# Kernel optimization log

Hardware: AMD Instinct MI355X
Metric: run time of the kernel (lower is better)

The kernel has to match this reference:

```python
import jax, jax.numpy as jnp
from jax import lax
import numpy as np

EPS = 1e-5

def _bn(x, g, b, m, v):
    # inference-mode BatchNorm2d over channel dim (NCHW)
    scale = (g * lax.rsqrt(v + EPS))[None, :, None, None]
    return (x - m[None, :, None, None]) * scale + b[None, :, None, None]

def _conv(x, w, dil, pad):
    return lax.conv_general_dilated(
        x, w, window_strides=(1, 1), padding=[(pad, pad), (pad, pad)],
        rhs_dilation=(dil, dil), dimension_numbers=('NCHW', 'OIHW', 'NCHW'))

def _interleave(b0, b1, b2, b3):
    # out[2i+r, 2j+c] = branch[2r+c][i, j]  (equivalent to the mask*nearest-upsample trick)
    bs, C, H, W = b0.shape
    row0 = jnp.stack([b0, b1], axis=-1)          # (bs,C,H,W,2) -> c
    row1 = jnp.stack([b2, b3], axis=-1)
    s = jnp.stack([row0, row1], axis=-2)          # (bs,C,H,W,2,2) -> (...,r,c)
    return s.transpose(0, 1, 2, 4, 3, 5).reshape(bs, C, 2 * H, 2 * W)

def setup_inputs() -> dict:
    key = jax.random.key(0)
    ks = iter(jax.random.split(key, 40))
    B, Cin, Cout, H = 8, 256, 128, 64
    inp = {"x": jax.random.normal(next(ks), (B, Cin, H, H), jnp.float32)}
    inp["w0"] = jax.random.normal(next(ks), (Cout, Cin, 1, 1), jnp.float32) * 0.05
    for i in (1, 2, 3):
        inp[f"w{i}"] = jax.random.normal(next(ks), (Cout, Cin, 3, 3), jnp.float32) * 0.02
    inp["wp"] = jax.random.normal(next(ks), (Cout, Cout, 1, 1), jnp.float32) * 0.05
    for t in ("0", "1", "2", "3", "p"):
        inp[f"g{t}"] = 1.0 + 0.1 * jax.random.normal(next(ks), (Cout,), jnp.float32)
        inp[f"b{t}"] = 0.1 * jax.random.normal(next(ks), (Cout,), jnp.float32)
        inp[f"m{t}"] = 0.05 * jax.random.normal(next(ks), (Cout,), jnp.float32)
        inp[f"v{t}"] = jax.random.uniform(next(ks), (Cout,), jnp.float32, 0.5, 1.5)
    return inp

def reference(x, w0, w1, w2, w3, wp,
              g0, b0, m0, v0, g1, b1, m1, v1,
              g2, b2, m2, v2, g3, b3, m3, v3,
              gp, bp, mp, vp):
    RATES = (6, 12, 18)
    br0 = jax.nn.relu(_bn(_conv(x, w0, 1, 0), g0, b0, m0, v0))
    br1 = jax.nn.relu(_bn(_conv(x, w1, RATES[0], RATES[0]), g1, b1, m1, v1))
    br2 = jax.nn.relu(_bn(_conv(x, w2, RATES[1], RATES[1]), g2, b2, m2, v2))
    br3 = jax.nn.relu(_bn(_conv(x, w3, RATES[2], RATES[2]), g3, b3, m3, v3))
    up = _interleave(br0, br1, br2, br3)          # (B, Cout, 2H, 2W)
    return jax.nn.relu(_bn(_conv(up, wp, 1, 0), gp, bp, mp, vp))  # dropout: eval identity
```

## Files before the change

### kernel.cpp

```cpp
#include <hip/hip_runtime.h>
#include <stdint.h>

typedef unsigned int uint32;
typedef uint16_t u16;
typedef short short8 __attribute__((ext_vector_type(8)));
typedef short shortx4 __attribute__((ext_vector_type(4)));
typedef float floatx4 __attribute__((ext_vector_type(4)));

#define BN_EPS 1e-5f

#define XROW 25600
#define XPLANE 1638400
#define XB_SHORTS 13107200
#define ZROW_SHORTS 25600

#define OFF0 0
#define OFF1 32768
#define OFF2 327680
#define OFF3 622592
#define OFFP 917504
#define WPK_SHORTS 933888
#define U_B0 4096
#define U_B  36864
#define U_TOT 116736

__device__ __forceinline__ u16 f2bf(float f) {
  uint32 u = __float_as_uint(f);
  u += 0x7fffu + ((u >> 16) & 1u);
  return (u16)(u >> 16);
}

__global__ void k_xcvt(const float* __restrict__ x, u16* __restrict__ xb) {
  int bid = blockIdx.x, tid = threadIdx.x;
  if (bid == 512) {
    uint32* z = (uint32*)(xb + XB_SHORTS);
    #pragma unroll
    for (int r = 0; r < 50; ++r) z[r * 256 + tid] = 0;
    return;
  }
  int n = bid >> 6, i = bid & 63;
  uint32* rw = (uint32*)(xb + (size_t)n * XPLANE + (size_t)i * XROW);
  #pragma unroll
  for (int e = 0; e < 18; ++e) {
    int idx = e * 256 + tid;
    int colid = idx >> 7;
    int jp = (colid < 18) ? colid : (colid + 64);
    rw[jp * 128 + (idx & 127)] = 0;
  }
  int ci2 = tid & 127, jh = tid >> 7;
  const float* xs = x + ((size_t)(n * 256 + 2 * ci2) * 64 + i) * 64 + jh * 32;
  #pragma unroll 4
  for (int j = 0; j < 32; ++j) {
    float f0 = xs[j];
    float f1 = xs[4096 + j];
    uint32 pk = (uint32)f2bf(f0) | ((uint32)f2bf(f1) << 16);
    rw[(jh * 32 + j + 18) * 128 + ci2] = pk;
  }
}

__global__ void k_wpack(const float* __restrict__ w0, const float* __restrict__ w1,
                        const float* __restrict__ w2, const float* __restrict__ w3,
                        const float* __restrict__ wp, u16* __restrict__ wpk) {
  int g = blockIdx.x * 256 + threadIdx.x;
  if (g >= U_TOT) return;
  const float* w; int Cin, t, q, u, off; bool k3;
  if (g < U_B0) {
    int blk = g >> 10; w = w0; Cin = 256; k3 = false; t = 0; q = blk; u = g & 1023;
    off = OFF0 + blk * 8192;
  } else if (g < U_B0 + U_B) {
    int g1 = g - U_B0; int blk = g1 >> 10; w = w1; Cin = 256; k3 = true;
    t = blk >> 2; q = blk & 3; u = g1 & 1023; off = OFF1 + blk * 8192;
  } else if (g < U_B0 + 2*U_B) {
    int g1 = g - (U_B0 + U_B); int blk = g1 >> 10; w = w2; Cin = 256; k3 = true;
    t = blk >> 2; q = blk & 3; u = g1 & 1023; off = OFF2 + blk * 8192;
  } else if (g < U_B0 + 3*U_B) {
    int g1 = g - (U_B0 + 2*U_B); int blk = g1 >> 10; w = w3; Cin = 256; k3 = true;
    t = blk >> 2; q = blk & 3; u = g1 & 1023; off = OFF3 + blk * 8192;
  } else {
    int g1 = g - (U_B0 + 3*U_B); int blk = g1 >> 10; w = wp; Cin = 128; k3 = false;
    t = 0; q = blk; u = g1 & 1023; off = OFFP + blk * 8192;
  }
  int co = u >> 3, slot = u & 7;
  int sl = slot ^ (co & 7);
  int ci0 = q * 64 + sl * 8;
  int kh = k3 ? (t / 3) : 0, kw = k3 ? (t % 3) : 0;
  union { short8 s; u16 us[8]; } v;
  #pragma unroll
  for (int e = 0; e < 8; ++e) {
    int ci = ci0 + e;
    float wv = k3 ? w[((co * Cin + ci) * 3 + kh) * 3 + kw] : w[co * Cin + ci];
    v.us[e] = f2bf(wv);
  }
  *(short8*)(wpk + off + u * 8) = v.s;
}

__global__ void k_bn(const float* g0,const float* b0,const float* m0,const float* v0,
                     const float* g1,const float* b1,const float* m1,const float* v1,
                     const float* g2,const float* b2,const float* m2,const float* v2,
                     const float* g3,const float* b3,const float* m3,const float* v3,
                     const float* gp,const float* bp,const float* mp,const float* vp,
                     float* __restrict__ bn) {
  int i = blockIdx.x * 256 + threadIdx.x;
  if (i >= 640) return;
  int t = i >> 7, co = i & 127;
  const float *G, *B, *M, *V;
  if      (t == 0) { G=g0; B=b0; M=m0; V=v0; }
  else if (t == 1) { G=g1; B=b1; M=m1; V=v1; }
  else if (t == 2) { G=g2; B=b2; M=m2; V=v2; }
  else if (t == 3) { G=g3; B=b3; M=m3; V=v3; }
  else             { G=gp; B=bp; M=mp; V=vp; }
  float s = G[co] * rsqrtf(V[co] + BN_EPS);
  bn[t * 256 + co]       = s;
  bn[t * 256 + 128 + co] = B[co] - M[co] * s;
}

__global__ __launch_bounds__(256, 3)
void k_main(const u16* __restrict__ xb, const u16* __restrict__ wpk,
            const float* __restrict__ bn, float* __restrict__ out) {
  __shared__ __align__(16) u16 As[8192];
  __shared__ __align__(16) u16 BP[16384];

  int tid = threadIdx.x;
  int bid = blockIdx.x;
  int n = bid & 7;
  int rest = bid >> 3;
  int tile = rest >> 2;
  int b = (rest ^ (rest >> 5)) & 3;
  int i0 = tile * 2;
  int lane = tid & 63, wid = tid >> 6;
  int wm = wid >> 1, wn = wid & 1;
  int m16 = lane & 15, hh = lane >> 4;

  const u16* xg = xb + (size_t)n * XPLANE;
  const u16* zr = xb + XB_SHORTS;
  int d = (b == 0) ? 0 : ((b == 1) ? 6 : ((b == 2) ? 12 : 18));
  int NS = ((b == 0) ? 1 : 9) * 4;
  int woff8 = ((b == 0) ? OFF0 : (b == 1) ? OFF1 : (b == 2) ? OFF2 : OFF3) / 8;

  const short8* wpk8 = (const short8*)wpk;
  short8* AsS8 = (short8*)As;
  short8* BsS8 = (short8*)BP;
  const short8* PsS8 = (const short8*)BP;

  floatx4 acc[4][4];
  #pragma unroll
  for (int a1 = 0; a1 < 4; ++a1)
    #pragma unroll
    for (int a2 = 0; a2 < 4; ++a2) acc[a1][a2] = (floatx4){0.f, 0.f, 0.f, 0.f};

  short8 ra[4];
  short8 rb[4];
  int cg = tid & 7, pxo = tid >> 3;

  auto prefetch = [&](int s) {
    int abase = woff8 + s * 1024;
    #pragma unroll
    for (int w = 0; w < 4; ++w) ra[w] = wpk8[abase + w * 256 + tid];
    int t = s >> 2, q = s & 3;
    int di = d * (t / 3 - 1);
    int dj = d * (t % 3 - 1);
    #pragma unroll
    for (int k = 0; k < 4; ++k) {
      int px = k * 32 + pxo;
      int ii = i0 + (k >> 1) + di;
      const u16* base = (ii >= 0 && ii < 64) ? (xg + ii * XROW) : zr;
      int jj = (px & 63) + 18 + dj;
      rb[k] = *(const short8*)(base + jj * 256 + q * 64 + cg * 8);
    }
  };

  prefetch(0);

  for (int s = 0; s < NS; ++s) {
    __builtin_amdgcn_s_barrier();
    #pragma unroll
    for (int w = 0; w < 4; ++w) AsS8[w * 256 + tid] = ra[w];
    #pragma unroll
    for (int k = 0; k < 4; ++k) {
      int px = k * 32 + pxo;
      BsS8[px * 8 + (cg ^ (px & 7))] = rb[k];
    }
    if (s + 1 < NS) prefetch(s + 1);
    asm volatile("s_waitcnt lgkmcnt(0)" ::: "memory");
    __builtin_amdgcn_s_barrier();
    __builtin_amdgcn_sched_barrier(0);
    #pragma unroll
    for (int kk = 0; kk < 2; ++kk) {
      short8 af[4], bfr[4];
      #pragma unroll
      for (int f = 0; f < 4; ++f) {
        int row = wm * 64 + f * 16 + m16;
        af[f] = AsS8[row * 8 + ((kk * 4 + hh) ^ (row & 7))];
      }
      #pragma unroll
      for (int f = 0; f < 4; ++f) {
        int px = wn * 64 + f * 16 + m16;
        bfr[f] = BsS8[px * 8 + ((kk * 4 + hh) ^ (px & 7))];
      }
      #pragma unroll
      for (int fm = 0; fm < 4; ++fm)
        #pragma unroll
        for (int fn = 0; fn < 4; ++fn)
          acc[fm][fn] = __builtin_amdgcn_mfma_f32_16x16x32_bf16(
              af[fm], bfr[fn], acc[fm][fn], 0, 0, 0);
    }
  }

  __syncthreads();
  #pragma unroll
  for (int fm = 0; fm < 4; ++fm) {
    int co_base = wm * 64 + fm * 16 + hh * 4;
    float sc[4], sh[4];
    #pragma unroll
    for (int r = 0; r < 4; ++r) {
      sc[r] = bn[b * 256 + co_base + r];
      sh[r] = bn[b * 256 + 128 + co_base + r];
    }
    #pragma unroll
    for (int fn = 0; fn < 4; ++fn) {
      int px = wn * 64 + fn * 16 + m16;
      int sw = (px >> 1) & 7;
      int slot = (co_base >> 3) ^ sw;
      union { shortx4 s4; u16 us[4]; } pk;
      #pragma unroll
      for (int r = 0; r < 4; ++r)
        pk.us[r] = f2bf(fmaxf(acc[fm][fn][r] * sc[r] + sh[r], 0.f));
      *(shortx4*)&BP[px * 128 + slot * 8 + (co_base & 7)] = pk.s4;
    }
  }

  floatx4 acc2[4][4];
  #pragma unroll
  for (int a1 = 0; a1 < 4; ++a1)
    #pragma unroll
    for (int a2 = 0; a2 < 4; ++a2) acc2[a1][a2] = (floatx4){0.f, 0.f, 0.f, 0.f};

  for (int q = 0; q < 2; ++q) {
    if (q == 1) __syncthreads();
    int abase = OFFP / 8 + q * 1024;
    #pragma unroll
    for (int w = 0; w < 4; ++w) AsS8[w * 256 + tid] = wpk8[abase + w * 256 + tid];
    __syncthreads();
    #pragma unroll
    for (int kk = 0; kk < 2; ++kk) {
      short8 af[4], bfr[4];
      #pragma unroll
      for (int f = 0; f < 4; ++f) {
        int row = wm * 64 + f * 16 + m16;
        af[f] = AsS8[row * 8 + ((kk * 4 + hh) ^ (row & 7))];
      }
      #pragma unroll
      for (int f = 0; f < 4; ++f) {
        int px = wn * 64 + f * 16 + m16;
        int slot = q * 8 + kk * 4 + hh;
        bfr[f] = PsS8[px * 16 + (slot ^ ((px >> 1) & 7))];
      }
      #pragma unroll
      for (int fm = 0; fm < 4; ++fm)
        #pragma unroll
        for (int fn = 0; fn < 4; ++fn)
          acc2[fm][fn] = __builtin_amdgcn_mfma_f32_16x16x32_bf16(
              af[fm], bfr[fn], acc2[fm][fn], 0, 0, 0);
    }
  }

  int rb2 = b >> 1, cb = b & 1;
  #pragma unroll
  for (int fm = 0; fm < 4; ++fm) {
    #pragma unroll
    for (int r = 0; r < 4; ++r) {
      int co = wm * 64 + fm * 16 + hh * 4 + r;
      float s  = bn[1024 + co];
      float sh = bn[1024 + 128 + co];
      #pragma unroll
      for (int fn = 0; fn < 4; ++fn) {
        int px = wn * 64 + fn * 16 + m16;
        int i = i0 + (px >> 6), j = px & 63;
        float v = fmaxf(acc2[fm][fn][r] * s + sh, 0.f);
        out[(((n * 128 + co) * 128) + (2 * i + rb2)) * 128 + (2 * j + cb)] = v;
      }
    }
  }
}

extern "C" void kernel_launch(void* const* d_in, const int* in_sizes, int n_in,
                              void* d_out, int out_size, void* d_ws, size_t ws_size,
                              hipStream_t stream) {
  const float* x  = (const float*)d_in[0];
  const float* w0 = (const float*)d_in[1];
  const float* w1 = (const float*)d_in[2];
  const float* w2 = (const float*)d_in[3];
  const float* w3 = (const float*)d_in[4];
  const float* wp = (const float*)d_in[5];

  u16* xbuf = (u16*)d_ws;
  u16* wpk  = (u16*)d_ws + (XB_SHORTS + ZROW_SHORTS);
  float* bn = (float*)((char*)d_ws + (size_t)(XB_SHORTS + ZROW_SHORTS + WPK_SHORTS) * 2);

  k_xcvt<<<513, 256, 0, stream>>>(x, xbuf);
  k_wpack<<<456, 256, 0, stream>>>(w0, w1, w2, w3, wp, wpk);
  k_bn<<<3, 256, 0, stream>>>(
      (const float*)d_in[6],  (const float*)d_in[7],  (const float*)d_in[8],  (const float*)d_in[9],
      (const float*)d_in[10], (const float*)d_in[11], (const float*)d_in[12], (const float*)d_in[13],
      (const float*)d_in[14], (const float*)d_in[15], (const float*)d_in[16], (const float*)d_in[17],
      (const float*)d_in[18], (const float*)d_in[19], (const float*)d_in[20], (const float*)d_in[21],
      (const float*)d_in[22], (const float*)d_in[23], (const float*)d_in[24], (const float*)d_in[25],
      bn);
  k_main<<<1024, 256, 0, stream>>>(xbuf, wpk, bn, (float*)d_out);
}
```

Before: 109.2 us.

## Load weight MFMA fragments directly from global memory, dropping the LDS A tile

The weight packing layout changes to slot-major order so each lane can fetch its MFMA A fragments straight from global memory (L2-resident weights). The A operand no longer goes through LDS in either the conv GEMM loop or the projection GEMM, which removes the LDS As buffer, its stores and reads, and some barriers. This frees 16KB of LDS, which could raise occupancy. In exchange the global weight loads are issued inside the loop without a full stage of prefetch, so latency may be exposed. The sched_barrier is also removed.

```diff
diff --git a/kernel.cpp b/kernel.cpp
--- a/kernel.cpp
+++ b/kernel.cpp
@@ -80,9 +80,8 @@
     int g1 = g - (U_B0 + 3*U_B); int blk = g1 >> 10; w = wp; Cin = 128; k3 = false;
     t = 0; q = blk; u = g1 & 1023; off = OFFP + blk * 8192;
   }
-  int co = u >> 3, slot = u & 7;
-  int sl = slot ^ (co & 7);
-  int ci0 = q * 64 + sl * 8;
+  int slot = u >> 7, co = u & 127;
+  int ci0 = q * 64 + slot * 8;
   int kh = k3 ? (t / 3) : 0, kw = k3 ? (t % 3) : 0;
   union { short8 s; u16 us[8]; } v;
   #pragma unroll
@@ -117,7 +116,6 @@
 __global__ __launch_bounds__(256, 3)
 void k_main(const u16* __restrict__ xb, const u16* __restrict__ wpk,
             const float* __restrict__ bn, float* __restrict__ out) {
-  __shared__ __align__(16) u16 As[8192];
   __shared__ __align__(16) u16 BP[16384];
 
   int tid = threadIdx.x;
@@ -138,7 +136,6 @@
   int woff8 = ((b == 0) ? OFF0 : (b == 1) ? OFF1 : (b == 2) ? OFF2 : OFF3) / 8;
 
   const short8* wpk8 = (const short8*)wpk;
-  short8* AsS8 = (short8*)As;
   short8* BsS8 = (short8*)BP;
   const short8* PsS8 = (const short8*)BP;
 
@@ -148,14 +145,11 @@
     #pragma unroll
     for (int a2 = 0; a2 < 4; ++a2) acc[a1][a2] = (floatx4){0.f, 0.f, 0.f, 0.f};
 
-  short8 ra[4];
   short8 rb[4];
   int cg = tid & 7, pxo = tid >> 3;
-
-  auto prefetch = [&](int s) {
-    int abase = woff8 + s * 1024;
-    #pragma unroll
-    for (int w = 0; w < 4; ++w) ra[w] = wpk8[abase + w * 256 + tid];
+  int arow = wm * 64 + m16;
+
+  auto prefetchB = [&](int s) {
     int t = s >> 2, q = s & 3;
     int di = d * (t / 3 - 1);
     int dj = d * (t % 3 - 1);
@@ -169,29 +163,30 @@
     }
   };
 
-  prefetch(0);
+  prefetchB(0);
 
   for (int s = 0; s < NS; ++s) {
     __builtin_amdgcn_s_barrier();
-    #pragma unroll
-    for (int w = 0; w < 4; ++w) AsS8[w * 256 + tid] = ra[w];
     #pragma unroll
     for (int k = 0; k < 4; ++k) {
       int px = k * 32 + pxo;
       BsS8[px * 8 + (cg ^ (px & 7))] = rb[k];
     }
-    if (s + 1 < NS) prefetch(s + 1);
+    short8 af[2][4];
+    {
+      int abase = woff8 + s * 1024;
+      #pragma unroll
+      for (int kk = 0; kk < 2; ++kk)
+        #pragma unroll
+        for (int f = 0; f < 4; ++f)
+          af[kk][f] = wpk8[abase + (kk * 4 + hh) * 128 + arow + f * 16];
+    }
+    if (s + 1 < NS) prefetchB(s + 1);
     asm volatile("s_waitcnt lgkmcnt(0)" ::: "memory");
     __builtin_amdgcn_s_barrier();
-    __builtin_amdgcn_sched_barrier(0);
     #pragma unroll
     for (int kk = 0; kk < 2; ++kk) {
-      short8 af[4], bfr[4];
-      #pragma unroll
-      for (int f = 0; f < 4; ++f) {
-        int row = wm * 64 + f * 16 + m16;
-        af[f] = AsS8[row * 8 + ((kk * 4 + hh) ^ (row & 7))];
-      }
+      short8 bfr[4];
       #pragma unroll
       for (int f = 0; f < 4; ++f) {
         int px = wn * 64 + f * 16 + m16;
@@ -202,7 +197,7 @@
         #pragma unroll
         for (int fn = 0; fn < 4; ++fn)
           acc[fm][fn] = __builtin_amdgcn_mfma_f32_16x16x32_bf16(
-              af[fm], bfr[fn], acc[fm][fn], 0, 0, 0);
+              af[kk][fm], bfr[fn], acc[fm][fn], 0, 0, 0);
     }
   }
 
@@ -235,20 +230,15 @@
     #pragma unroll
     for (int a2 = 0; a2 < 4; ++a2) acc2[a1][a2] = (floatx4){0.f, 0.f, 0.f, 0.f};
 
+  __syncthreads();
+  #pragma unroll
   for (int q = 0; q < 2; ++q) {
-    if (q == 1) __syncthreads();
-    int abase = OFFP / 8 + q * 1024;
-    #pragma unroll
-    for (int w = 0; w < 4; ++w) AsS8[w * 256 + tid] = wpk8[abase + w * 256 + tid];
-    __syncthreads();
     #pragma unroll
     for (int kk = 0; kk < 2; ++kk) {
-      short8 af[4], bfr[4];
-      #pragma unroll
-      for (int f = 0; f < 4; ++f) {
-        int row = wm * 64 + f * 16 + m16;
-        af[f] = AsS8[row * 8 + ((kk * 4 + hh) ^ (row & 7))];
-      }
+      short8 af2[4], bfr[4];
+      #pragma unroll
+      for (int f = 0; f < 4; ++f)
+        af2[f] = wpk8[OFFP / 8 + q * 1024 + (kk * 4 + hh) * 128 + arow + f * 16];
       #pragma unroll
       for (int f = 0; f < 4; ++f) {
         int px = wn * 64 + f * 16 + m16;
@@ -260,7 +250,7 @@
         #pragma unroll
         for (int fn = 0; fn < 4; ++fn)
           acc2[fm][fn] = __builtin_amdgcn_mfma_f32_16x16x32_bf16(
-              af[fm], bfr[fn], acc2[fm][fn], 0, 0, 0);
+              af2[fm], bfr[fn], acc2[fm][fn], 0, 0, 0);
     }
   }
 
```

Result: faster. 104.3 us (-4.5%).
